# Kernel tuning notes

Measured on AMD Instinct MI355X. Metric: run time of the kernel, lower is better.

The kernel has to match this reference:

```python
import jax, jax.numpy as jnp
import numpy as np

B, T, D = 64, 256, 1024
H, HID, WIN, DH = 4, 512, 9, 256
EPS = 1e-7


def _expmap0(e):
    # Lorentz expmap at origin (k=1) of tangent vector [0, e]
    n = jnp.maximum(jnp.linalg.norm(e, axis=-1, keepdims=True), EPS)
    return jnp.concatenate([jnp.cosh(n), jnp.sinh(n) * e / n], axis=-1)


def _logmap0(p):
    y0 = jnp.maximum(p[..., :1], 1.0 + EPS)
    ys = p[..., 1:]
    ns = jnp.maximum(jnp.linalg.norm(ys, axis=-1, keepdims=True), EPS)
    d = jnp.log(y0 + jnp.sqrt(y0 * y0 - 1.0))  # arccosh
    return d * ys / ns


def _lorentz_dist(p):
    # d(x,y) = arccosh(-<x,y>_L), with F.threshold(.,1,1) floor like the torch code
    g = jnp.concatenate([-p[..., :1], p[..., 1:]], axis=-1)
    inner = -jnp.einsum('bid,bjd->bij', g, p)
    y = jnp.where(inner > 1.0, inner, 1.0)
    dist = jnp.log(y + jnp.sqrt(jnp.maximum(y * y - 1.0, EPS)))
    return jnp.clip(dist, 1e-6, 200.0)


def _forward(x, c_x, w_loc, b_loc, Wq, bq, Wk, bk, Wv, bv, Wo, bo, Wc1, bc1,
             Wg1, bg1, Wg2, bg2, ln_g, ln_b, Wl1, bl1, Wcls, bcls, seq_len):
    idx = jnp.arange(T)
    dmat = jnp.abs(idx[:, None] - idx[None, :]).astype(x.dtype)           # [T,T]
    adj_loc = jnp.exp(-jnp.abs(w_loc * dmat * dmat - b_loc))              # DistanceAdj_PEL
    off = idx[None, :] - idx[:, None]
    band = (off >= -(WIN // 2)) & (off <= WIN - 1 - WIN // 2)             # get_mask window band

    # --- TCA: local-window multi-head attention with distance-adjacency bias ---
    q = (x @ Wq + bq).reshape(B, T, H, HID // H)
    k = (x @ Wk + bk).reshape(B, T, H, HID // H)
    v = (x @ Wv + bv).reshape(B, T, H, HID // H)
    att = jnp.einsum('bihd,bjhd->bhij', q, k) / jnp.sqrt(jnp.asarray(D, x.dtype)) + adj_loc
    att = jnp.where(band, att, -1e9)
    att = jax.nn.softmax(att, axis=-1)
    o = jnp.einsum('bhij,bjhd->bihd', att, v).reshape(B, T, HID) @ Wo + bo
    x = x + o
    x = jax.nn.relu(x @ Wc1 + bc1)                                        # conv1d k=1 == pointwise linear
    x = jnp.concatenate([x, c_x], axis=-1)                                # [B,T,1024]

    disadj = jnp.exp(-dmat / jnp.exp(jnp.asarray(1.0, x.dtype)))          # temporal DistanceAdj
    proj = _expmap0(x)                                                    # [B,T,1025] Lorentz point

    # --- lorentz-distance adjacency, per-sample ragged threshold + softmax ---
    a = jnp.exp(-_lorentz_dist(proj))
    thr = jnp.where(a > 0.8, a, 0.0)                                      # F.threshold(.,0.8,0)
    valid = idx[None, :] < seq_len[:, None]                               # [B,T]
    logits = jnp.where(valid[:, None, :], thr, -jnp.inf)
    adj_h = jax.nn.softmax(logits, axis=-1)                               # softmax over valid cols
    adj_h = jnp.where(valid[:, None, :] & valid[:, :, None], adj_h, 0.0)

    # --- two hyperbolic GCN encoders (tangent-space linear + neighborhood agg) ---
    h = _logmap0(proj)                                                    # [B,T,1024]
    x1 = jax.nn.leaky_relu(jnp.einsum('bij,bjd->bid', adj_h, h @ Wg1 + bg1))
    x2 = jax.nn.leaky_relu(jnp.einsum('ij,bjd->bid', disadj, h @ Wg2 + bg2))
    xc = jnp.concatenate([x1, x2], axis=-1)                               # [B,T,512]

    mu = jnp.mean(xc, axis=-1, keepdims=True)
    var = jnp.var(xc, axis=-1, keepdims=True)
    xn = (xc - mu) / jnp.sqrt(var + 1e-5) * ln_g + ln_b                   # LayerNorm(512)
    xt = jax.nn.gelu(xn @ Wl1 + bl1, approximate=False)                   # linear1 (conv k=1) + gelu
    x_e = jax.nn.sigmoid(xt @ Wcls + bcls)                                # HypClassifier -> [B,T,1]
    return x_e, jnp.transpose(xt, (0, 2, 1))                              # (x_e, x[B,512,T])


def setup_inputs() -> dict:
    key = jax.random.key(0)
    ks = jax.random.split(key, 16)
    w = lambda i, shp: jax.random.normal(ks[i], shp, jnp.float32) * 0.02
    inp = {
        'x': jax.random.normal(ks[0], (B, T, D), jnp.float32) * 0.05,
        'c_x': jax.random.normal(ks[1], (B, T, D // 2), jnp.float32) * 0.05,
        'w_loc': jnp.asarray(0.6, jnp.float32),
        'b_loc': jnp.asarray(0.2, jnp.float32),
        'Wq': w(2, (D, HID)), 'bq': jnp.zeros((HID,), jnp.float32),
        'Wk': w(3, (D, HID)), 'bk': jnp.zeros((HID,), jnp.float32),
        'Wv': w(4, (D, HID)), 'bv': jnp.zeros((HID,), jnp.float32),
        'Wo': w(5, (HID, D)), 'bo': jnp.zeros((D,), jnp.float32),
        'Wc1': w(6, (D, D // 2)), 'bc1': jnp.zeros((D // 2,), jnp.float32),
        'Wg1': w(7, (D, DH)), 'bg1': jnp.zeros((DH,), jnp.float32),
        'Wg2': w(8, (D, DH)), 'bg2': jnp.zeros((DH,), jnp.float32),
        'ln_g': jnp.ones((512,), jnp.float32), 'ln_b': jnp.zeros((512,), jnp.float32),
        'Wl1': w(9, (512, 512)), 'bl1': jnp.zeros((512,), jnp.float32),
        'Wcls': w(10, (512, 1)), 'bcls': jnp.zeros((1,), jnp.float32),
        'seq_len': jax.random.randint(ks[11], (B,), T // 2, T + 1).astype(jnp.int32),
    }
    return inp


def reference(x, c_x, w_loc, b_loc, Wq, bq, Wk, bk, Wv, bv, Wo, bo, Wc1, bc1,
              Wg1, bg1, Wg2, bg2, ln_g, ln_b, Wl1, bl1, Wcls, bcls, seq_len):
    return _forward(x, c_x, w_loc, b_loc, Wq, bq, Wk, bk, Wv, bv, Wo, bo, Wc1, bc1,
                    Wg1, bg1, Wg2, bg2, ln_g, ln_b, Wl1, bl1, Wcls, bcls, seq_len)
```

## Files before the change

### kernel.cpp

```cpp
#include <hip/hip_runtime.h>
#include <hip/hip_bf16.h>
#include <math.h>

enum { M_NONE=0, M_RELU=1, M_GELU=2, M_RESID=3, M_ROWSCALE=4 };

typedef __hip_bfloat16 bf16;
typedef short s8v __attribute__((ext_vector_type(8)));
typedef float f4v __attribute__((ext_vector_type(4)));

__device__ __forceinline__ void gload16(const bf16* g, short* l) {
  __builtin_amdgcn_global_load_lds(
      (const __attribute__((address_space(1))) void*)g,
      (__attribute__((address_space(3))) void*)l, 16, 0, 0);
}

__global__ __launch_bounds__(256)
void transK(const float* __restrict__ src, bf16* __restrict__ dst,
            int N, int rowOff, int dstLd)
{
  __shared__ float tile[32][33];
  int k0 = blockIdx.y * 32, n0 = blockIdx.x * 32;
  int tx = threadIdx.x, ty = threadIdx.y;
#pragma unroll
  for (int i = 0; i < 4; i++)
    tile[ty + i * 8][tx] = src[(size_t)(k0 + ty + i * 8) * N + n0 + tx];
  __syncthreads();
#pragma unroll
  for (int i = 0; i < 4; i++)
    dst[(size_t)(n0 + ty + i * 8 + rowOff) * dstLd + k0 + tx] =
        __float2bfloat16(tile[tx][ty + i * 8]);
}

__global__ __launch_bounds__(256)
void conv_x(const float* __restrict__ src, bf16* __restrict__ dst, int n4)
{
  for (int i = blockIdx.x * 256 + threadIdx.x; i < n4; i += gridDim.x * 256) {
    float4 v = *(const float4*)&src[(size_t)i * 4];
    dst[(size_t)i * 4 + 0] = __float2bfloat16(v.x);
    dst[(size_t)i * 4 + 1] = __float2bfloat16(v.y);
    dst[(size_t)i * 4 + 2] = __float2bfloat16(v.z);
    dst[(size_t)i * 4 + 3] = __float2bfloat16(v.w);
  }
}

__global__ void pack_bias(const float* bq, const float* bk, const float* bv,
                          const float* bg1, const float* bg2,
                          float* bqkv, float* bgg)
{
  int t = blockIdx.x * 256 + threadIdx.x;
  if (t < 512) bqkv[t] = bq[t];
  else if (t < 1024) bqkv[t] = bk[t - 512];
  else if (t < 1536) bqkv[t] = bv[t - 1024];
  else if (t < 1792) bgg[t - 1536] = bg1[t - 1536];
  else if (t < 2048) bgg[t - 1792 + 256] = bg2[t - 1792];
}

template<int MODE, int OUTB>
__global__ __launch_bounds__(256)
void gemm_nt(const bf16* __restrict__ A, const bf16* __restrict__ Bt,
             const float* __restrict__ bias, const float* __restrict__ aux,
             float* __restrict__ Cf, bf16* __restrict__ Cb,
             int K, int ldC, int ldAux)
{
  __shared__ short As[128 * 32];
  __shared__ short Bs[128 * 32];
  const int tid = threadIdx.x;
  const int m0 = blockIdx.y * 128, n0 = blockIdx.x * 128;
  const int w = tid >> 6, l = tid & 63;
  const int wr = w >> 1, wc = w & 1;
  const int lr = l & 15, lk = l >> 4;
  const int srow = l >> 2, sslot = l & 3;

  f4v acc[4][4];
#pragma unroll
  for (int m = 0; m < 4; m++)
#pragma unroll
    for (int n = 0; n < 4; n++) acc[m][n] = (f4v){0.f, 0.f, 0.f, 0.f};

  for (int kt = 0; kt < K; kt += 32) {
#pragma unroll
    for (int q = 0; q < 2; q++) {
      int seg = q * 4 + w;
      int r = seg * 16 + srow;
      int c = sslot ^ ((r >> 1) & 3);
      gload16(&A[(size_t)(m0 + r) * K + kt + c * 8], &As[seg * 512]);
      gload16(&Bt[(size_t)(n0 + r) * K + kt + c * 8], &Bs[seg * 512]);
    }
    __syncthreads();
    s8v af[4], bfr[4];
#pragma unroll
    for (int m = 0; m < 4; m++) {
      int row = wr * 64 + m * 16 + lr;
      af[m] = *(const s8v*)&As[row * 32 + ((lk ^ ((row >> 1) & 3)) * 8)];
      int col = wc * 64 + m * 16 + lr;
      bfr[m] = *(const s8v*)&Bs[col * 32 + ((lk ^ ((col >> 1) & 3)) * 8)];
    }
#pragma unroll
    for (int m = 0; m < 4; m++)
#pragma unroll
      for (int n = 0; n < 4; n++)
        acc[m][n] = __builtin_amdgcn_mfma_f32_16x16x32_bf16(af[m], bfr[n], acc[m][n], 0, 0, 0);
    __syncthreads();
  }

#pragma unroll
  for (int m = 0; m < 4; m++) {
#pragma unroll
    for (int reg = 0; reg < 4; reg++) {
      int grow = m0 + wr * 64 + m * 16 + lk * 4 + reg;
      float rs = (MODE == M_ROWSCALE) ? aux[grow] : 1.f;
#pragma unroll
      for (int n = 0; n < 4; n++) {
        int gcol = n0 + wc * 64 + n * 16 + lr;
        float v = acc[m][n][reg];
        if (MODE == M_ROWSCALE) v *= rs;
        v += bias[gcol];
        if (MODE == M_RELU) v = fmaxf(v, 0.f);
        if (MODE == M_GELU) v = 0.5f * v * (1.f + erff(v * 0.70710678118654752f));
        if (MODE == M_RESID) v += aux[(size_t)grow * ldAux + gcol];
        if (OUTB) Cb[(size_t)grow * ldC + gcol] = __float2bfloat16(v);
        else      Cf[(size_t)grow * ldC + gcol] = v;
      }
    }
  }
}

__global__ __launch_bounds__(256)
void gemm_pp(const bf16* __restrict__ P, const float* __restrict__ p0,
             float* __restrict__ thr)
{
  __shared__ short As[128 * 32];
  __shared__ short Bs[128 * 32];
  const int tid = threadIdx.x;
  const int b = blockIdx.z;
  const int m0 = blockIdx.y * 128, n0 = blockIdx.x * 128;
  const bf16* Pb = P + (size_t)b * 256 * 1024;
  const int w = tid >> 6, l = tid & 63;
  const int wr = w >> 1, wc = w & 1;
  const int lr = l & 15, lk = l >> 4;
  const int srow = l >> 2, sslot = l & 3;

  f4v acc[4][4];
#pragma unroll
  for (int m = 0; m < 4; m++)
#pragma unroll
    for (int n = 0; n < 4; n++) acc[m][n] = (f4v){0.f, 0.f, 0.f, 0.f};

  for (int kt = 0; kt < 1024; kt += 32) {
#pragma unroll
    for (int q = 0; q < 2; q++) {
      int seg = q * 4 + w;
      int r = seg * 16 + srow;
      int c = sslot ^ ((r >> 1) & 3);
      gload16(&Pb[(size_t)(m0 + r) * 1024 + kt + c * 8], &As[seg * 512]);
      gload16(&Pb[(size_t)(n0 + r) * 1024 + kt + c * 8], &Bs[seg * 512]);
    }
    __syncthreads();
    s8v af[4], bfr[4];
#pragma unroll
    for (int m = 0; m < 4; m++) {
      int row = wr * 64 + m * 16 + lr;
      af[m] = *(const s8v*)&As[row * 32 + ((lk ^ ((row >> 1) & 3)) * 8)];
      int col = wc * 64 + m * 16 + lr;
      bfr[m] = *(const s8v*)&Bs[col * 32 + ((lk ^ ((col >> 1) & 3)) * 8)];
    }
#pragma unroll
    for (int m = 0; m < 4; m++)
#pragma unroll
      for (int n = 0; n < 4; n++)
        acc[m][n] = __builtin_amdgcn_mfma_f32_16x16x32_bf16(af[m], bfr[n], acc[m][n], 0, 0, 0);
    __syncthreads();
  }

  const float* p0b = p0 + b * 256;
#pragma unroll
  for (int m = 0; m < 4; m++) {
#pragma unroll
    for (int reg = 0; reg < 4; reg++) {
      int gr = m0 + wr * 64 + m * 16 + lk * 4 + reg;
      float pi = p0b[gr];
#pragma unroll
      for (int n = 0; n < 4; n++) {
        int gc = n0 + wc * 64 + n * 16 + lr;
        float inner = pi * p0b[gc] - acc[m][n][reg];
        float y = fmaxf(inner, 1.f);
        float d = logf(y + sqrtf(fmaxf(y * y - 1.f, 1e-7f)));
        d = fminf(fmaxf(d, 1e-6f), 200.f);
        float a = expf(-d);
        thr[((size_t)(b * 256 + gr)) * 256 + gc] = (a > 0.8f) ? a : 0.f;
      }
    }
  }
}

__global__ __launch_bounds__(256)
void band_attn(const bf16* __restrict__ qkv, const float* __restrict__ wlp,
               const float* __restrict__ blp, bf16* __restrict__ o)
{
  int flat = blockIdx.x * 4 + (threadIdx.x >> 6);
  int l = threadIdx.x & 63;
  int h = flat & 3, i = (flat >> 2) & 255, b = flat >> 10;
  const float wl = wlp[0], bl = blp[0];
  size_t rq = ((size_t)(b * 256 + i)) * 1536 + h * 128 + l;
  float q0 = __bfloat162float(qkv[rq]), q1 = __bfloat162float(qkv[rq + 64]);
  float att[9];
#pragma unroll
  for (int jj = 0; jj < 9; jj++) {
    int j = i - 4 + jj;
    float val = -1e30f;
    if (j >= 0 && j < 256) {
      size_t rk = ((size_t)(b * 256 + j)) * 1536 + h * 128 + l + 512;
      float p = q0 * __bfloat162float(qkv[rk]) + q1 * __bfloat162float(qkv[rk + 64]);
#pragma unroll
      for (int s = 32; s; s >>= 1) p += __shfl_xor(p, s);
      float dd = fabsf((float)(i - j));
      float adj = expf(-fabsf(wl * dd * dd - bl));
      val = p * 0.03125f + adj;
    }
    att[jj] = val;
  }
  float m = att[0];
#pragma unroll
  for (int jj = 1; jj < 9; jj++) m = fmaxf(m, att[jj]);
  float p[9], sum = 0.f;
#pragma unroll
  for (int jj = 0; jj < 9; jj++) { p[jj] = expf(att[jj] - m); sum += p[jj]; }
  float inv = 1.f / sum;
  float o0 = 0.f, o1 = 0.f;
#pragma unroll
  for (int jj = 0; jj < 9; jj++) {
    int j = i - 4 + jj;
    if (j >= 0 && j < 256) {
      size_t rv = ((size_t)(b * 256 + j)) * 1536 + h * 128 + l + 1024;
      float wgt = p[jj] * inv;
      o0 += wgt * __bfloat162float(qkv[rv]);
      o1 += wgt * __bfloat162float(qkv[rv + 64]);
    }
  }
  size_t ro = ((size_t)(b * 256 + i)) * 512 + h * 128 + l;
  o[ro] = __float2bfloat16(o0);
  o[ro + 64] = __float2bfloat16(o1);
}

__global__ __launch_bounds__(256)
void rownorm_proj(const float* __restrict__ xcat, const float* __restrict__ cx,
                  bf16* __restrict__ Pb, float* __restrict__ p0,
                  float* __restrict__ alpha)
{
  int row = blockIdx.x;
  int t = threadIdx.x;
  float4 e;
  if (t < 128) e = *(const float4*)&xcat[(size_t)row * 512 + t * 4];
  else         e = *(const float4*)&cx[(size_t)row * 512 + (t - 128) * 4];
  float s = e.x * e.x + e.y * e.y + e.z * e.z + e.w * e.w;
#pragma unroll
  for (int o = 32; o; o >>= 1) s += __shfl_xor(s, o);
  __shared__ float red[4];
  if ((t & 63) == 0) red[t >> 6] = s;
  __syncthreads();
  float tot = red[0] + red[1] + red[2] + red[3];
  float n = fmaxf(sqrtf(tot), 1e-7f);
  float ch = coshf(n), sh = sinhf(n);
  float sc = sh / n;
  float4 pr; pr.x = sc * e.x; pr.y = sc * e.y; pr.z = sc * e.z; pr.w = sc * e.w;
  size_t po = (size_t)row * 1024 + t * 4;
  Pb[po + 0] = __float2bfloat16(pr.x);
  Pb[po + 1] = __float2bfloat16(pr.y);
  Pb[po + 2] = __float2bfloat16(pr.z);
  Pb[po + 3] = __float2bfloat16(pr.w);
  float s2 = pr.x * pr.x + pr.y * pr.y + pr.z * pr.z + pr.w * pr.w;
#pragma unroll
  for (int o = 32; o; o >>= 1) s2 += __shfl_xor(s2, o);
  __syncthreads();
  if ((t & 63) == 0) red[t >> 6] = s2;
  __syncthreads();
  float tot2 = red[0] + red[1] + red[2] + red[3];
  if (t == 0) {
    float ns = fmaxf(sqrtf(tot2), 1e-7f);
    float y0 = fmaxf(ch, 1.f + 1e-7f);
    float d = logf(y0 + sqrtf(y0 * y0 - 1.f));
    p0[row] = ch;
    alpha[row] = d / ns;
  }
}

__global__ __launch_bounds__(256)
void adj_softmax_apply(const float* __restrict__ thr, const float* __restrict__ G,
                       const int* __restrict__ seq_len, float* __restrict__ xc)
{
  __shared__ float Sb[32][260];
  __shared__ float Bp[16][260];
  const int tid = threadIdx.x;
  const int ty = tid >> 4, tx = tid & 15;
  const int i0 = blockIdx.x * 32;
  const int b = blockIdx.y;
  const int sl = seq_len[b];

  float acc[2][16];
#pragma unroll
  for (int r = 0; r < 2; r++)
#pragma unroll
    for (int m = 0; m < 4; m++) {
      float4 t4 = *(const float4*)&thr[((size_t)(b * 256 + i0 + ty * 2 + r)) * 256 + m * 64 + tx * 4];
      acc[r][m*4+0] = t4.x; acc[r][m*4+1] = t4.y;
      acc[r][m*4+2] = t4.z; acc[r][m*4+3] = t4.w;
    }

  float mx[2] = {-1e30f, -1e30f};
#pragma unroll
  for (int r = 0; r < 2; r++)
#pragma unroll
    for (int m = 0; m < 4; m++)
#pragma unroll
      for (int q = 0; q < 4; q++) {
        int idx = m * 4 + q;
        int c = m * 64 + tx * 4 + q;
        float lg = (c < sl) ? acc[r][idx] : -1e30f;
        acc[r][idx] = lg;
        mx[r] = fmaxf(mx[r], lg);
      }
#pragma unroll
  for (int o = 1; o < 16; o <<= 1) {
    mx[0] = fmaxf(mx[0], __shfl_xor(mx[0], o));
    mx[1] = fmaxf(mx[1], __shfl_xor(mx[1], o));
  }
  float sm[2] = {0.f, 0.f};
#pragma unroll
  for (int r = 0; r < 2; r++)
#pragma unroll
    for (int idx = 0; idx < 16; idx++) {
      float e = (acc[r][idx] > -1e29f) ? expf(acc[r][idx] - mx[r]) : 0.f;
      acc[r][idx] = e; sm[r] += e;
    }
#pragma unroll
  for (int o = 1; o < 16; o <<= 1) {
    sm[0] += __shfl_xor(sm[0], o);
    sm[1] += __shfl_xor(sm[1], o);
  }
  float inv[2] = {1.f / sm[0], 1.f / sm[1]};
  bool vi[2] = { (i0 + ty * 2) < sl, (i0 + ty * 2 + 1) < sl };
#pragma unroll
  for (int r = 0; r < 2; r++)
#pragma unroll
    for (int m = 0; m < 4; m++) {
      float4 s4;
      s4.x = vi[r] ? acc[r][m*4+0] * inv[r] : 0.f;
      s4.y = vi[r] ? acc[r][m*4+1] * inv[r] : 0.f;
      s4.z = vi[r] ? acc[r][m*4+2] * inv[r] : 0.f;
      s4.w = vi[r] ? acc[r][m*4+3] * inv[r] : 0.f;
      *(float4*)&Sb[ty * 2 + r][m * 64 + tx * 4] = s4;
    }
  __syncthreads();

  float acc2[2][16];
#pragma unroll
  for (int r = 0; r < 2; r++)
#pragma unroll
    for (int j = 0; j < 16; j++) acc2[r][j] = 0.f;

  for (int jt = 0; jt < 256; jt += 16) {
#pragma unroll
    for (int rep = 0; rep < 4; rep++) {
      int f = tid + rep * 256;
      int jl = f >> 6, c4 = (f & 63) << 2;
      *(float4*)&Bp[jl][c4] = *(const float4*)&G[(size_t)(b * 256 + jt + jl) * 512 + c4];
    }
    __syncthreads();
#pragma unroll
    for (int jj = 0; jj < 16; jj++) {
      float s0 = Sb[ty * 2][jt + jj];
      float s1 = Sb[ty * 2 + 1][jt + jj];
      float4 bm[4];
#pragma unroll
      for (int m = 0; m < 4; m++) bm[m] = *(const float4*)&Bp[jj][m * 64 + tx * 4];
#pragma unroll
      for (int m = 0; m < 4; m++) {
        acc2[0][m*4+0] = fmaf(s0, bm[m].x, acc2[0][m*4+0]);
        acc2[0][m*4+1] = fmaf(s0, bm[m].y, acc2[0][m*4+1]);
        acc2[0][m*4+2] = fmaf(s0, bm[m].z, acc2[0][m*4+2]);
        acc2[0][m*4+3] = fmaf(s0, bm[m].w, acc2[0][m*4+3]);
        acc2[1][m*4+0] = fmaf(s1, bm[m].x, acc2[1][m*4+0]);
        acc2[1][m*4+1] = fmaf(s1, bm[m].y, acc2[1][m*4+1]);
        acc2[1][m*4+2] = fmaf(s1, bm[m].z, acc2[1][m*4+2]);
        acc2[1][m*4+3] = fmaf(s1, bm[m].w, acc2[1][m*4+3]);
      }
    }
    __syncthreads();
  }
#pragma unroll
  for (int r = 0; r < 2; r++)
#pragma unroll
    for (int m = 0; m < 4; m++) {
      float4 o4;
      float v0 = acc2[r][m*4+0], v1 = acc2[r][m*4+1], v2 = acc2[r][m*4+2], v3 = acc2[r][m*4+3];
      o4.x = v0 > 0.f ? v0 : 0.01f * v0;
      o4.y = v1 > 0.f ? v1 : 0.01f * v1;
      o4.z = v2 > 0.f ? v2 : 0.01f * v2;
      o4.w = v3 > 0.f ? v3 : 0.01f * v3;
      *(float4*)&xc[(size_t)(b * 256 + i0 + ty * 2 + r) * 512 + m * 64 + tx * 4] = o4;
    }

  const float INV_E = 0.36787944117144233f;
#pragma unroll
  for (int r = 0; r < 2; r++)
#pragma unroll
    for (int j = 0; j < 16; j++) acc2[r][j] = 0.f;

  for (int jt = 0; jt < 256; jt += 16) {
#pragma unroll
    for (int rep = 0; rep < 4; rep++) {
      int f = tid + rep * 256;
      int jl = f >> 6, c4 = (f & 63) << 2;
      *(float4*)&Bp[jl][c4] = *(const float4*)&G[(size_t)(b * 256 + jt + jl) * 512 + 256 + c4];
    }
    __syncthreads();
#pragma unroll
    for (int jj = 0; jj < 16; jj++) {
      int j = jt + jj;
      float d0 = expf(-fabsf((float)(i0 + ty * 2 - j)) * INV_E);
      float d1 = expf(-fabsf((float)(i0 + ty * 2 + 1 - j)) * INV_E);
      float4 bm[4];
#pragma unroll
      for (int m = 0; m < 4; m++) bm[m] = *(const float4*)&Bp[jj][m * 64 + tx * 4];
#pragma unroll
      for (int m = 0; m < 4; m++) {
        acc2[0][m*4+0] = fmaf(d0, bm[m].x, acc2[0][m*4+0]);
        acc2[0][m*4+1] = fmaf(d0, bm[m].y, acc2[0][m*4+1]);
        acc2[0][m*4+2] = fmaf(d0, bm[m].z, acc2[0][m*4+2]);
        acc2[0][m*4+3] = fmaf(d0, bm[m].w, acc2[0][m*4+3]);
        acc2[1][m*4+0] = fmaf(d1, bm[m].x, acc2[1][m*4+0]);
        acc2[1][m*4+1] = fmaf(d1, bm[m].y, acc2[1][m*4+1]);
        acc2[1][m*4+2] = fmaf(d1, bm[m].z, acc2[1][m*4+2]);
        acc2[1][m*4+3] = fmaf(d1, bm[m].w, acc2[1][m*4+3]);
      }
    }
    __syncthreads();
  }
#pragma unroll
  for (int r = 0; r < 2; r++)
#pragma unroll
    for (int m = 0; m < 4; m++) {
      float4 o4;
      float v0 = acc2[r][m*4+0], v1 = acc2[r][m*4+1], v2 = acc2[r][m*4+2], v3 = acc2[r][m*4+3];
      o4.x = v0 > 0.f ? v0 : 0.01f * v0;
      o4.y = v1 > 0.f ? v1 : 0.01f * v1;
      o4.z = v2 > 0.f ? v2 : 0.01f * v2;
      o4.w = v3 > 0.f ? v3 : 0.01f * v3;
      *(float4*)&xc[(size_t)(b * 256 + i0 + ty * 2 + r) * 512 + 256 + m * 64 + tx * 4] = o4;
    }
}

__global__ __launch_bounds__(256)
void layernorm_k(const float* __restrict__ xc, const float* __restrict__ g,
                 const float* __restrict__ bta, bf16* __restrict__ out)
{
  int row = blockIdx.x * 4 + (threadIdx.x >> 6);
  int l = threadIdx.x & 63;
  const float* r = xc + (size_t)row * 512;
  float v[8];
  float s = 0.f;
#pragma unroll
  for (int q = 0; q < 8; q++) { v[q] = r[l + 64 * q]; s += v[q]; }
#pragma unroll
  for (int o = 32; o; o >>= 1) s += __shfl_xor(s, o);
  float mu = s * (1.f / 512.f);
  float s2 = 0.f;
#pragma unroll
  for (int q = 0; q < 8; q++) { float d = v[q] - mu; s2 += d * d; }
#pragma unroll
  for (int o = 32; o; o >>= 1) s2 += __shfl_xor(s2, o);
  float var = s2 * (1.f / 512.f);
  float inv = 1.f / sqrtf(var + 1e-5f);
#pragma unroll
  for (int q = 0; q < 8; q++) {
    int c = l + 64 * q;
    out[(size_t)row * 512 + c] = __float2bfloat16((v[q] - mu) * inv * g[c] + bta[c]);
  }
}

__global__ __launch_bounds__(256)
void xe_kernel(const float* __restrict__ xt, const float* __restrict__ Wcls,
               const float* __restrict__ bcls, float* __restrict__ out)
{
  int row = blockIdx.x * 4 + (threadIdx.x >> 6);
  int l = threadIdx.x & 63;
  float s = 0.f;
#pragma unroll
  for (int q = 0; q < 8; q++) {
    int c = l + 64 * q;
    s += xt[(size_t)row * 512 + c] * Wcls[c];
  }
#pragma unroll
  for (int o = 32; o; o >>= 1) s += __shfl_xor(s, o);
  if (l == 0) out[row] = 1.f / (1.f + expf(-(s + bcls[0])));
}

__global__ void transpose_xt(const float* __restrict__ xt, float* __restrict__ out)
{
  __shared__ float tile[32][33];
  int b = blockIdx.z;
  int t0 = blockIdx.x * 32, d0 = blockIdx.y * 32;
  int tx = threadIdx.x, ty = threadIdx.y;
#pragma unroll
  for (int i = 0; i < 4; i++)
    tile[ty + i * 8][tx] = xt[((size_t)(b * 256) + t0 + ty + i * 8) * 512 + d0 + tx];
  __syncthreads();
#pragma unroll
  for (int i = 0; i < 4; i++)
    out[((size_t)(b * 512) + d0 + ty + i * 8) * 256 + t0 + tx] = tile[tx][ty + i * 8];
}

extern "C" void kernel_launch(void* const* d_in, const int* in_sizes, int n_in,
                              void* d_out, int out_size, void* d_ws, size_t ws_size,
                              hipStream_t stream) {
  (void)in_sizes; (void)n_in; (void)out_size; (void)ws_size;
  const float* x     = (const float*)d_in[0];
  const float* c_x   = (const float*)d_in[1];
  const float* w_loc = (const float*)d_in[2];
  const float* b_loc = (const float*)d_in[3];
  const float* Wq    = (const float*)d_in[4];
  const float* bq    = (const float*)d_in[5];
  const float* Wk    = (const float*)d_in[6];
  const float* bk    = (const float*)d_in[7];
  const float* Wv    = (const float*)d_in[8];
  const float* bv    = (const float*)d_in[9];
  const float* Wo    = (const float*)d_in[10];
  const float* bo    = (const float*)d_in[11];
  const float* Wc1   = (const float*)d_in[12];
  const float* bc1   = (const float*)d_in[13];
  const float* Wg1   = (const float*)d_in[14];
  const float* bg1   = (const float*)d_in[15];
  const float* Wg2   = (const float*)d_in[16];
  const float* bg2   = (const float*)d_in[17];
  const float* ln_g  = (const float*)d_in[18];
  const float* ln_b  = (const float*)d_in[19];
  const float* Wl1   = (const float*)d_in[20];
  const float* bl1   = (const float*)d_in[21];
  const float* Wcls  = (const float*)d_in[22];
  const float* bcls  = (const float*)d_in[23];
  const int*   seq_len = (const int*)d_in[24];

  float* ws = (float*)d_ws;
  bf16*  xb    = (bf16*)ws;
  bf16*  x2b   = (bf16*)ws;
  float* G1G2  = ws;
  bf16*  xnb   = (bf16*)ws;
  bf16*  qkvb  = (bf16*)(ws + 8388608);
  float* xcat  = ws + 8388608;
  bf16*  Pb    = (bf16*)(ws + 16777216);
  float* thr   = ws + 25165824;
  float* xt    = ws + 25165824;
  bf16*  ob    = (bf16*)(ws + 33554432);
  float* xc    = ws + 37748736;
  bf16*  WqkvT = (bf16*)(ws + 46137344);
  bf16*  WoT   = (bf16*)(ws + 46923776);
  bf16*  Wc1T  = (bf16*)(ws + 47185920);
  bf16*  Wg12T = (bf16*)(ws + 47448064);
  bf16*  Wl1T  = (bf16*)(ws + 47710208);
  float* bqkv  = ws + 47841280;
  float* bgg   = ws + 47842816;
  float* p0    = ws + 47843328;
  float* alpha = ws + 47859712;

  dim3 blk(256);
  dim3 tblk(32, 8);
  transK<<<dim3(16, 32), tblk, 0, stream>>>(Wq,  WqkvT, 512,    0, 1024);
  transK<<<dim3(16, 32), tblk, 0, stream>>>(Wk,  WqkvT, 512,  512, 1024);
  transK<<<dim3(16, 32), tblk, 0, stream>>>(Wv,  WqkvT, 512, 1024, 1024);
  transK<<<dim3(32, 16), tblk, 0, stream>>>(Wo,  WoT, 1024,    0,  512);
  transK<<<dim3(16, 32), tblk, 0, stream>>>(Wc1, Wc1T, 512,    0, 1024);
  transK<<<dim3( 8, 32), tblk, 0, stream>>>(Wg1, Wg12T, 256,   0, 1024);
  transK<<<dim3( 8, 32), tblk, 0, stream>>>(Wg2, Wg12T, 256, 256, 1024);
  transK<<<dim3(16, 16), tblk, 0, stream>>>(Wl1, Wl1T, 512,    0,  512);
  conv_x<<<2048, blk, 0, stream>>>(x, xb, 4194304);
  pack_bias<<<8, blk, 0, stream>>>(bq, bk, bv, bg1, bg2, bqkv, bgg);

  gemm_nt<M_NONE, 1><<<dim3(12, 128), blk, 0, stream>>>(xb, WqkvT, bqkv, nullptr, nullptr, qkvb, 1024, 1536, 0);
  band_attn<<<16384, blk, 0, stream>>>(qkvb, w_loc, b_loc, ob);
  gemm_nt<M_RESID, 1><<<dim3(8, 128), blk, 0, stream>>>(ob, WoT, bo, x, nullptr, x2b, 512, 1024, 1024);
  gemm_nt<M_RELU, 0><<<dim3(4, 128), blk, 0, stream>>>(x2b, Wc1T, bc1, nullptr, xcat, nullptr, 1024, 512, 0);
  rownorm_proj<<<16384, blk, 0, stream>>>(xcat, c_x, Pb, p0, alpha);
  gemm_nt<M_ROWSCALE, 0><<<dim3(4, 128), blk, 0, stream>>>(Pb, Wg12T, bgg, alpha, G1G2, nullptr, 1024, 512, 0);
  gemm_pp<<<dim3(2, 2, 64), blk, 0, stream>>>(Pb, p0, thr);
  adj_softmax_apply<<<dim3(8, 64), blk, 0, stream>>>(thr, G1G2, seq_len, xc);
  layernorm_k<<<4096, blk, 0, stream>>>(xc, ln_g, ln_b, xnb);
  gemm_nt<M_GELU, 0><<<dim3(4, 128), blk, 0, stream>>>(xnb, Wl1T, bl1, nullptr, xt, nullptr, 512, 512, 0);
  float* out = (float*)d_out;
  xe_kernel<<<4096, blk, 0, stream>>>(xt, Wcls, bcls, out);
  transpose_xt<<<dim3(8, 16, 64), tblk, 0, stream>>>(xt, out + 16384);
}
```

Measured before the change: 651.2 us.

## Move adjacency-apply matmuls to bf16 MFMA with transposed G output

```diff
diff --git a/kernel.cpp b/kernel.cpp
--- a/kernel.cpp
+++ b/kernel.cpp
@@ -2,11 +2,21 @@
 #include <hip/hip_bf16.h>
 #include <math.h>
 
-enum { M_NONE=0, M_RELU=1, M_GELU=2, M_RESID=3, M_ROWSCALE=4 };
+enum { M_NONE=0, M_RELU=1, M_GELU=2, M_RESID=3, M_ROWSCALE=4, M_GT=5 };
 
 typedef __hip_bfloat16 bf16;
 typedef short s8v __attribute__((ext_vector_type(8)));
+typedef short s4v __attribute__((ext_vector_type(4)));
 typedef float f4v __attribute__((ext_vector_type(4)));
+
+__device__ __forceinline__ short f2bf(float v) {
+  bf16 h = __float2bfloat16(v);
+  return *reinterpret_cast<short*>(&h);
+}
+__device__ __forceinline__ float bf2f(short s) {
+  bf16 h = *reinterpret_cast<bf16*>(&s);
+  return __bfloat162float(h);
+}
 
 __device__ __forceinline__ void gload16(const bf16* g, short* l) {
   __builtin_amdgcn_global_load_lds(
@@ -109,15 +119,20 @@
     for (int reg = 0; reg < 4; reg++) {
       int grow = m0 + wr * 64 + m * 16 + lk * 4 + reg;
       float rs = (MODE == M_ROWSCALE) ? aux[grow] : 1.f;
+      float rb = (MODE == M_GT) ? bias[grow] : 0.f;
 #pragma unroll
       for (int n = 0; n < 4; n++) {
         int gcol = n0 + wc * 64 + n * 16 + lr;
         float v = acc[m][n][reg];
-        if (MODE == M_ROWSCALE) v *= rs;
-        v += bias[gcol];
-        if (MODE == M_RELU) v = fmaxf(v, 0.f);
-        if (MODE == M_GELU) v = 0.5f * v * (1.f + erff(v * 0.70710678118654752f));
-        if (MODE == M_RESID) v += aux[(size_t)grow * ldAux + gcol];
+        if (MODE == M_GT) {
+          v = v * aux[gcol] + rb;
+        } else {
+          if (MODE == M_ROWSCALE) v *= rs;
+          v += bias[gcol];
+          if (MODE == M_RELU) v = fmaxf(v, 0.f);
+          if (MODE == M_GELU) v = 0.5f * v * (1.f + erff(v * 0.70710678118654752f));
+          if (MODE == M_RESID) v += aux[(size_t)grow * ldAux + gcol];
+        }
         if (OUTB) Cb[(size_t)grow * ldC + gcol] = __float2bfloat16(v);
         else      Cf[(size_t)grow * ldC + gcol] = v;
       }
@@ -127,7 +142,7 @@
 
 __global__ __launch_bounds__(256)
 void gemm_pp(const bf16* __restrict__ P, const float* __restrict__ p0,
-             float* __restrict__ thr)
+             bf16* __restrict__ thr)
 {
   __shared__ short As[128 * 32];
   __shared__ short Bs[128 * 32];
@@ -187,7 +202,7 @@
         float d = logf(y + sqrtf(fmaxf(y * y - 1.f, 1e-7f)));
         d = fminf(fmaxf(d, 1e-6f), 200.f);
         float a = expf(-d);
-        thr[((size_t)(b * 256 + gr)) * 256 + gc] = (a > 0.8f) ? a : 0.f;
+        thr[((size_t)(b * 256 + gr)) * 256 + gc] = __float2bfloat16((a > 0.8f) ? a : 0.f);
       }
     }
   }
@@ -285,27 +300,31 @@
 }
 
 __global__ __launch_bounds__(256)
-void adj_softmax_apply(const float* __restrict__ thr, const float* __restrict__ G,
-                       const int* __restrict__ seq_len, float* __restrict__ xc)
-{
-  __shared__ float Sb[32][260];
-  __shared__ float Bp[16][260];
+void adj_apply(const bf16* __restrict__ thr, const bf16* __restrict__ Gt,
+               const int* __restrict__ seq_len, float* __restrict__ xc)
+{
+  __shared__ short Sb[32 * 264];
+  __shared__ short Bst[4 * 256 * 8];
   const int tid = threadIdx.x;
   const int ty = tid >> 4, tx = tid & 15;
   const int i0 = blockIdx.x * 32;
-  const int b = blockIdx.y;
+  const int b  = blockIdx.y;
   const int sl = seq_len[b];
+  const int w = tid >> 6, l = tid & 63;
+  const int lr = l & 15, lk = l >> 4;
+  const float INV_E = 0.36787944117144233f;
 
   float acc[2][16];
 #pragma unroll
-  for (int r = 0; r < 2; r++)
+  for (int r = 0; r < 2; r++) {
+    const short* trow = (const short*)(thr + ((size_t)(b * 256 + i0 + ty * 2 + r)) * 256);
 #pragma unroll
     for (int m = 0; m < 4; m++) {
-      float4 t4 = *(const float4*)&thr[((size_t)(b * 256 + i0 + ty * 2 + r)) * 256 + m * 64 + tx * 4];
-      acc[r][m*4+0] = t4.x; acc[r][m*4+1] = t4.y;
-      acc[r][m*4+2] = t4.z; acc[r][m*4+3] = t4.w;
-    }
-
+      s4v t4 = *(const s4v*)&trow[m * 64 + tx * 4];
+      acc[r][m*4+0] = bf2f(t4[0]); acc[r][m*4+1] = bf2f(t4[1]);
+      acc[r][m*4+2] = bf2f(t4[2]); acc[r][m*4+3] = bf2f(t4[3]);
+    }
+  }
   float mx[2] = {-1e30f, -1e30f};
 #pragma unroll
   for (int r = 0; r < 2; r++)
@@ -343,111 +362,73 @@
   for (int r = 0; r < 2; r++)
 #pragma unroll
     for (int m = 0; m < 4; m++) {
-      float4 s4;
-      s4.x = vi[r] ? acc[r][m*4+0] * inv[r] : 0.f;
-      s4.y = vi[r] ? acc[r][m*4+1] * inv[r] : 0.f;
-      s4.z = vi[r] ? acc[r][m*4+2] * inv[r] : 0.f;
-      s4.w = vi[r] ? acc[r][m*4+3] * inv[r] : 0.f;
-      *(float4*)&Sb[ty * 2 + r][m * 64 + tx * 4] = s4;
+      s4v s4;
+#pragma unroll
+      for (int q = 0; q < 4; q++)
+        s4[q] = f2bf(vi[r] ? acc[r][m*4+q] * inv[r] : 0.f);
+      *(s4v*)&Sb[(ty * 2 + r) * 264 + m * 64 + tx * 4] = s4;
     }
   __syncthreads();
 
-  float acc2[2][16];
-#pragma unroll
-  for (int r = 0; r < 2; r++)
-#pragma unroll
-    for (int j = 0; j < 16; j++) acc2[r][j] = 0.f;
-
-  for (int jt = 0; jt < 256; jt += 16) {
-#pragma unroll
-    for (int rep = 0; rep < 4; rep++) {
-      int f = tid + rep * 256;
-      int jl = f >> 6, c4 = (f & 63) << 2;
-      *(float4*)&Bp[jl][c4] = *(const float4*)&G[(size_t)(b * 256 + jt + jl) * 512 + c4];
-    }
+  for (int pass = 0; pass < 2; ++pass) {
+    const int nOff = pass * 256;
+    f4v a2[2][4];
+#pragma unroll
+    for (int m = 0; m < 2; m++)
+#pragma unroll
+      for (int n = 0; n < 4; n++) a2[m][n] = (f4v){0.f, 0.f, 0.f, 0.f};
+
+    for (int kt = 0; kt < 256; kt += 32) {
+      s8v breg[4];
+      const size_t gbase = (size_t)(nOff + tid) * 16384 + b * 256 + kt;
+#pragma unroll
+      for (int rch = 0; rch < 4; rch++)
+        breg[rch] = *(const s8v*)&((const short*)Gt)[gbase + rch * 8];
+      __syncthreads();
+#pragma unroll
+      for (int rch = 0; rch < 4; rch++)
+        *(s8v*)&Bst[rch * 2048 + tid * 8] = breg[rch];
+      __syncthreads();
+
+      s8v af[2], bfr[4];
+#pragma unroll
+      for (int m = 0; m < 2; m++) {
+        if (pass == 0) {
+          af[m] = *(const s8v*)&Sb[(m * 16 + lr) * 264 + kt + lk * 8];
+        } else {
+          float ri = (float)(i0 + m * 16 + lr);
+#pragma unroll
+          for (int e = 0; e < 8; e++) {
+            float jv = (float)(kt + lk * 8 + e);
+            af[m][e] = f2bf(__expf(-fabsf(ri - jv) * INV_E));
+          }
+        }
+      }
+#pragma unroll
+      for (int n = 0; n < 4; n++)
+        bfr[n] = *(const s8v*)&Bst[lk * 2048 + (w * 64 + n * 16 + lr) * 8];
+#pragma unroll
+      for (int m = 0; m < 2; m++)
+#pragma unroll
+        for (int n = 0; n < 4; n++)
+          a2[m][n] = __builtin_amdgcn_mfma_f32_16x16x32_bf16(af[m], bfr[n], a2[m][n], 0, 0, 0);
+    }
+
+#pragma unroll
+    for (int m = 0; m < 2; m++)
+#pragma unroll
+      for (int reg = 0; reg < 4; reg++) {
+        size_t grow = (size_t)(b * 256 + i0 + m * 16 + lk * 4 + reg);
+#pragma unroll
+        for (int n = 0; n < 4; n++) {
+          int gcol = nOff + w * 64 + n * 16 + lr;
+          float v = a2[m][n][reg];
+          v = v > 0.f ? v : 0.01f * v;
+          xc[grow * 512 + gcol] = v;
+        }
+      }
     __syncthreads();
-#pragma unroll
-    for (int jj = 0; jj < 16; jj++) {
-      float s0 = Sb[ty * 2][jt + jj];
-      float s1 = Sb[ty * 2 + 1][jt + jj];
-      float4 bm[4];
-#pragma unroll
-      for (int m = 0; m < 4; m++) bm[m] = *(const float4*)&Bp[jj][m * 64 + tx * 4];
-#pragma unroll
-      for (int m = 0; m < 4; m++) {
-        acc2[0][m*4+0] = fmaf(s0, bm[m].x, acc2[0][m*4+0]);
-        acc2[0][m*4+1] = fmaf(s0, bm[m].y, acc2[0][m*4+1]);
-        acc2[0][m*4+2] = fmaf(s0, bm[m].z, acc2[0][m*4+2]);
-        acc2[0][m*4+3] = fmaf(s0, bm[m].w, acc2[0][m*4+3]);
-        acc2[1][m*4+0] = fmaf(s1, bm[m].x, acc2[1][m*4+0]);
-        acc2[1][m*4+1] = fmaf(s1, bm[m].y, acc2[1][m*4+1]);
-        acc2[1][m*4+2] = fmaf(s1, bm[m].z, acc2[1][m*4+2]);
-        acc2[1][m*4+3] = fmaf(s1, bm[m].w, acc2[1][m*4+3]);
-      }
-    }
-    __syncthreads();
-  }
-#pragma unroll
-  for (int r = 0; r < 2; r++)
-#pragma unroll
-    for (int m = 0; m < 4; m++) {
-      float4 o4;
-      float v0 = acc2[r][m*4+0], v1 = acc2[r][m*4+1], v2 = acc2[r][m*4+2], v3 = acc2[r][m*4+3];
-      o4.x = v0 > 0.f ? v0 : 0.01f * v0;
-      o4.y = v1 > 0.f ? v1 : 0.01f * v1;
-      o4.z = v2 > 0.f ? v2 : 0.01f * v2;
-      o4.w = v3 > 0.f ? v3 : 0.01f * v3;
-      *(float4*)&xc[(size_t)(b * 256 + i0 + ty * 2 + r) * 512 + m * 64 + tx * 4] = o4;
-    }
-
-  const float INV_E = 0.36787944117144233f;
-#pragma unroll
-  for (int r = 0; r < 2; r++)
-#pragma unroll
-    for (int j = 0; j < 16; j++) acc2[r][j] = 0.f;
-
-  for (int jt = 0; jt < 256; jt += 16) {
-#pragma unroll
-    for (int rep = 0; rep < 4; rep++) {
-      int f = tid + rep * 256;
-      int jl = f >> 6, c4 = (f & 63) << 2;
-      *(float4*)&Bp[jl][c4] = *(const float4*)&G[(size_t)(b * 256 + jt + jl) * 512 + 256 + c4];
-    }
-    __syncthreads();
-#pragma unroll
-    for (int jj = 0; jj < 16; jj++) {
-      int j = jt + jj;
-      float d0 = expf(-fabsf((float)(i0 + ty * 2 - j)) * INV_E);
-      float d1 = expf(-fabsf((float)(i0 + ty * 2 + 1 - j)) * INV_E);
-      float4 bm[4];
-#pragma unroll
-      for (int m = 0; m < 4; m++) bm[m] = *(const float4*)&Bp[jj][m * 64 + tx * 4];
-#pragma unroll
-      for (int m = 0; m < 4; m++) {
-        acc2[0][m*4+0] = fmaf(d0, bm[m].x, acc2[0][m*4+0]);
-        acc2[0][m*4+1] = fmaf(d0, bm[m].y, acc2[0][m*4+1]);
-        acc2[0][m*4+2] = fmaf(d0, bm[m].z, acc2[0][m*4+2]);
-        acc2[0][m*4+3] = fmaf(d0, bm[m].w, acc2[0][m*4+3]);
-        acc2[1][m*4+0] = fmaf(d1, bm[m].x, acc2[1][m*4+0]);
-        acc2[1][m*4+1] = fmaf(d1, bm[m].y, acc2[1][m*4+1]);
-        acc2[1][m*4+2] = fmaf(d1, bm[m].z, acc2[1][m*4+2]);
-        acc2[1][m*4+3] = fmaf(d1, bm[m].w, acc2[1][m*4+3]);
-      }
-    }
-    __syncthreads();
-  }
-#pragma unroll
-  for (int r = 0; r < 2; r++)
-#pragma unroll
-    for (int m = 0; m < 4; m++) {
-      float4 o4;
-      float v0 = acc2[r][m*4+0], v1 = acc2[r][m*4+1], v2 = acc2[r][m*4+2], v3 = acc2[r][m*4+3];
-      o4.x = v0 > 0.f ? v0 : 0.01f * v0;
-      o4.y = v1 > 0.f ? v1 : 0.01f * v1;
-      o4.z = v2 > 0.f ? v2 : 0.01f * v2;
-      o4.w = v3 > 0.f ? v3 : 0.01f * v3;
-      *(float4*)&xc[(size_t)(b * 256 + i0 + ty * 2 + r) * 512 + 256 + m * 64 + tx * 4] = o4;
-    }
+  }
 }
 
 __global__ __launch_bounds__(256)
@@ -543,12 +524,12 @@
   float* ws = (float*)d_ws;
   bf16*  xb    = (bf16*)ws;
   bf16*  x2b   = (bf16*)ws;
-  float* G1G2  = ws;
+  bf16*  Gtb   = (bf16*)ws;
   bf16*  xnb   = (bf16*)ws;
   bf16*  qkvb  = (bf16*)(ws + 8388608);
   float* xcat  = ws + 8388608;
   bf16*  Pb    = (bf16*)(ws + 16777216);
-  float* thr   = ws + 25165824;
+  bf16*  thrb  = (bf16*)(ws + 25165824);
   float* xt    = ws + 25165824;
   bf16*  ob    = (bf16*)(ws + 33554432);
   float* xc    = ws + 37748736;
@@ -580,9 +561,9 @@
   gemm_nt<M_RESID, 1><<<dim3(8, 128), blk, 0, stream>>>(ob, WoT, bo, x, nullptr, x2b, 512, 1024, 1024);
   gemm_nt<M_RELU, 0><<<dim3(4, 128), blk, 0, stream>>>(x2b, Wc1T, bc1, nullptr, xcat, nullptr, 1024, 512, 0);
   rownorm_proj<<<16384, blk, 0, stream>>>(xcat, c_x, Pb, p0, alpha);
-  gemm_nt<M_ROWSCALE, 0><<<dim3(4, 128), blk, 0, stream>>>(Pb, Wg12T, bgg, alpha, G1G2, nullptr, 1024, 512, 0);
-  gemm_pp<<<dim3(2, 2, 64), blk, 0, stream>>>(Pb, p0, thr);
-  adj_softmax_apply<<<dim3(8, 64), blk, 0, stream>>>(thr, G1G2, seq_len, xc);
+  gemm_nt<M_GT, 1><<<dim3(128, 4), blk, 0, stream>>>(Wg12T, Pb, bgg, alpha, nullptr, Gtb, 1024, 16384, 0);
+  gemm_pp<<<dim3(2, 2, 64), blk, 0, stream>>>(Pb, p0, thrb);
+  adj_apply<<<dim3(8, 64), blk, 0, stream>>>(thrb, Gtb, seq_len, xc);
   layernorm_k<<<4096, blk, 0, stream>>>(xc, ln_g, ln_b, xnb);
   gemm_nt<M_GELU, 0><<<dim3(4, 128), blk, 0, stream>>>(xnb, Wl1T, bl1, nullptr, xt, nullptr, 512, 512, 0);
   float* out = (float*)d_out;
```

After: 715.3 us. 1.1x slower.

## Double-buffer LDS tiles in bf16 GEMM kernels to overlap loads with MFMA

Applied to the files above, without the earlier changes.

```diff
diff --git a/kernel.cpp b/kernel.cpp
--- a/kernel.cpp
+++ b/kernel.cpp
@@ -62,8 +62,8 @@
              float* __restrict__ Cf, bf16* __restrict__ Cb,
              int K, int ldC, int ldAux)
 {
-  __shared__ short As[128 * 32];
-  __shared__ short Bs[128 * 32];
+  __shared__ short As0[128 * 32], Bs0[128 * 32];
+  __shared__ short As1[128 * 32], Bs1[128 * 32];
   const int tid = threadIdx.x;
   const int m0 = blockIdx.y * 128, n0 = blockIdx.x * 128;
   const int w = tid >> 6, l = tid & 63;
@@ -77,29 +77,40 @@
 #pragma unroll
     for (int n = 0; n < 4; n++) acc[m][n] = (f4v){0.f, 0.f, 0.f, 0.f};
 
-  for (int kt = 0; kt < K; kt += 32) {
+  auto STAGE = [&](short* Asb, short* Bsb, int kt) {
 #pragma unroll
     for (int q = 0; q < 2; q++) {
       int seg = q * 4 + w;
       int r = seg * 16 + srow;
       int c = sslot ^ ((r >> 1) & 3);
-      gload16(&A[(size_t)(m0 + r) * K + kt + c * 8], &As[seg * 512]);
-      gload16(&Bt[(size_t)(n0 + r) * K + kt + c * 8], &Bs[seg * 512]);
-    }
-    __syncthreads();
+      gload16(&A[(size_t)(m0 + r) * K + kt + c * 8], &Asb[seg * 512]);
+      gload16(&Bt[(size_t)(n0 + r) * K + kt + c * 8], &Bsb[seg * 512]);
+    }
+  };
+  auto COMPUTE = [&](const short* Asb, const short* Bsb) {
     s8v af[4], bfr[4];
 #pragma unroll
     for (int m = 0; m < 4; m++) {
       int row = wr * 64 + m * 16 + lr;
-      af[m] = *(const s8v*)&As[row * 32 + ((lk ^ ((row >> 1) & 3)) * 8)];
+      af[m] = *(const s8v*)&Asb[row * 32 + ((lk ^ ((row >> 1) & 3)) * 8)];
       int col = wc * 64 + m * 16 + lr;
-      bfr[m] = *(const s8v*)&Bs[col * 32 + ((lk ^ ((col >> 1) & 3)) * 8)];
+      bfr[m] = *(const s8v*)&Bsb[col * 32 + ((lk ^ ((col >> 1) & 3)) * 8)];
     }
 #pragma unroll
     for (int m = 0; m < 4; m++)
 #pragma unroll
       for (int n = 0; n < 4; n++)
         acc[m][n] = __builtin_amdgcn_mfma_f32_16x16x32_bf16(af[m], bfr[n], acc[m][n], 0, 0, 0);
+  };
+
+  STAGE(As0, Bs0, 0);
+  __syncthreads();
+  for (int kt = 0; kt < K; kt += 64) {
+    if (kt + 32 < K) STAGE(As1, Bs1, kt + 32);
+    COMPUTE(As0, Bs0);
+    __syncthreads();
+    if (kt + 64 < K) STAGE(As0, Bs0, kt + 64);
+    if (kt + 32 < K) COMPUTE(As1, Bs1);
     __syncthreads();
   }
 
@@ -129,8 +140,8 @@
 void gemm_pp(const bf16* __restrict__ P, const float* __restrict__ p0,
              float* __restrict__ thr)
 {
-  __shared__ short As[128 * 32];
-  __shared__ short Bs[128 * 32];
+  __shared__ short As0[128 * 32], Bs0[128 * 32];
+  __shared__ short As1[128 * 32], Bs1[128 * 32];
   const int tid = threadIdx.x;
   const int b = blockIdx.z;
   const int m0 = blockIdx.y * 128, n0 = blockIdx.x * 128;
@@ -146,29 +157,40 @@
 #pragma unroll
     for (int n = 0; n < 4; n++) acc[m][n] = (f4v){0.f, 0.f, 0.f, 0.f};
 
-  for (int kt = 0; kt < 1024; kt += 32) {
+  auto STAGE = [&](short* Asb, short* Bsb, int kt) {
 #pragma unroll
     for (int q = 0; q < 2; q++) {
       int seg = q * 4 + w;
       int r = seg * 16 + srow;
       int c = sslot ^ ((r >> 1) & 3);
-      gload16(&Pb[(size_t)(m0 + r) * 1024 + kt + c * 8], &As[seg * 512]);
-      gload16(&Pb[(size_t)(n0 + r) * 1024 + kt + c * 8], &Bs[seg * 512]);
-    }
-    __syncthreads();
+      gload16(&Pb[(size_t)(m0 + r) * 1024 + kt + c * 8], &Asb[seg * 512]);
+      gload16(&Pb[(size_t)(n0 + r) * 1024 + kt + c * 8], &Bsb[seg * 512]);
+    }
+  };
+  auto COMPUTE = [&](const short* Asb, const short* Bsb) {
     s8v af[4], bfr[4];
 #pragma unroll
     for (int m = 0; m < 4; m++) {
       int row = wr * 64 + m * 16 + lr;
-      af[m] = *(const s8v*)&As[row * 32 + ((lk ^ ((row >> 1) & 3)) * 8)];
+      af[m] = *(const s8v*)&Asb[row * 32 + ((lk ^ ((row >> 1) & 3)) * 8)];
       int col = wc * 64 + m * 16 + lr;
-      bfr[m] = *(const s8v*)&Bs[col * 32 + ((lk ^ ((col >> 1) & 3)) * 8)];
+      bfr[m] = *(const s8v*)&Bsb[col * 32 + ((lk ^ ((col >> 1) & 3)) * 8)];
     }
 #pragma unroll
     for (int m = 0; m < 4; m++)
 #pragma unroll
       for (int n = 0; n < 4; n++)
         acc[m][n] = __builtin_amdgcn_mfma_f32_16x16x32_bf16(af[m], bfr[n], acc[m][n], 0, 0, 0);
+  };
+
+  STAGE(As0, Bs0, 0);
+  __syncthreads();
+  for (int kt = 0; kt < 1024; kt += 64) {
+    if (kt + 32 < 1024) STAGE(As1, Bs1, kt + 32);
+    COMPUTE(As0, Bs0);
+    __syncthreads();
+    if (kt + 64 < 1024) STAGE(As0, Bs0, kt + 64);
+    if (kt + 32 < 1024) COMPUTE(As1, Bs1);
     __syncthreads();
   }
 
```

Result: no change. 646.1 us (-0.8%).
